# Performance work log

Measured on AMD Instinct MI355X. Metric: run time of the kernel, lower is better.

Reference implementation:

```python
import jax, jax.numpy as jnp
import numpy as np

D_MODEL, N_HEADS, D_LATENT = 1024, 16, 256
HEAD_DIM = D_MODEL // N_HEADS
B, T = 2, 2048


def apply_rope(x):
    # x: [B, T, H, D]
    Tn, D = x.shape[1], x.shape[3]
    inv_freq = 1.0 / (10000.0 ** (jnp.arange(0, D, 2, dtype=jnp.float32) / D))
    t = jnp.arange(Tn, dtype=jnp.float32)
    freqs = jnp.outer(t, inv_freq)               # [T, D/2]
    sin_f = jnp.sin(freqs)[None, :, None, :]
    cos_f = jnp.cos(freqs)[None, :, None, :]
    x1, x2 = jnp.split(x, 2, axis=-1)
    return jnp.concatenate([x1 * cos_f - x2 * sin_f,
                            x1 * sin_f + x2 * cos_f], axis=-1)


def setup_inputs() -> dict:
    key = jax.random.key(0)
    ks = jax.random.split(key, 5)
    s = lambda fan_in: 1.0 / np.sqrt(fan_in)
    return {
        "x": jax.random.normal(ks[0], (B, T, D_MODEL), jnp.float32),
        "Wq": jax.random.normal(ks[1], (D_MODEL, D_MODEL), jnp.float32) * s(D_MODEL),
        "bq": jnp.zeros((D_MODEL,), jnp.float32),
        "Wkv_down": jax.random.normal(ks[2], (D_MODEL, D_LATENT), jnp.float32) * s(D_MODEL),
        "bkv_down": jnp.zeros((D_LATENT,), jnp.float32),
        "Wkv_up": jax.random.normal(ks[3], (D_LATENT, 2 * D_MODEL), jnp.float32) * s(D_LATENT),
        "bkv_up": jnp.zeros((2 * D_MODEL,), jnp.float32),
        "Wo": jax.random.normal(ks[4], (D_MODEL, D_MODEL), jnp.float32) * s(D_MODEL),
        "bo": jnp.zeros((D_MODEL,), jnp.float32),
    }


def reference(x, Wq, bq, Wkv_down, bkv_down, Wkv_up, bkv_up, Wo, bo):
    Bn, Tn = x.shape[0], x.shape[1]
    q = x @ Wq + bq                              # [B, T, d_model]
    kv = (x @ Wkv_down + bkv_down) @ Wkv_up + bkv_up  # [B, T, 2*d_model]
    q = q.reshape(Bn, Tn, N_HEADS, HEAD_DIM)
    kv = kv.reshape(Bn, Tn, N_HEADS, 2 * HEAD_DIM)
    k, v = jnp.split(kv, 2, axis=-1)
    q = apply_rope(q)
    k = apply_rope(k)
    q = q.transpose(0, 2, 1, 3)                  # [B, H, T, D]
    k = k.transpose(0, 2, 1, 3)
    v = v.transpose(0, 2, 1, 3)

    att = jnp.einsum('bhqd,bhkd->bhqk', q, k) / jnp.sqrt(jnp.float32(HEAD_DIM))

    idx = jnp.arange(Tn, dtype=jnp.float32)
    dist_signed = idx[:, None] - idx[None, :]    # [T, T]
    log_sparse = -0.1 * jnp.log(jnp.abs(dist_signed) + 1.0)
    decay = jnp.exp(-jnp.maximum(dist_signed, 0.0) * 0.01)
    att = att + (log_sparse + jnp.log(decay + 1e-9))[None, None]
    att = jax.nn.softmax(att, axis=-1)
    out = jnp.einsum('bhqk,bhkd->bhqd', att, v)  # [B, H, T, D]

    # Infini/memory branch: mean-pooled single-slot attention
    memory_k = jnp.mean(k, axis=2, keepdims=True)  # [B, H, 1, D]
    memory_v = jnp.mean(v, axis=2, keepdims=True)
    memory_scores = jnp.einsum('bhqd,bhkd->bhqk', q, memory_k)  # [B, H, T, 1]
    infini_out = jax.nn.sigmoid(memory_scores) * memory_v       # [B, H, T, D]
    out = out + 0.2 * infini_out

    out = out.transpose(0, 2, 1, 3).reshape(Bn, Tn, D_MODEL)
    return out @ Wo + bo
```

## Files before the change

### kernel.cpp

```cpp
#include <hip/hip_runtime.h>
#include <hip/hip_bf16.h>

#define D_MODEL 1024
#define N_HEADS 16
#define HEAD_DIM 64
#define D_LATENT 256
#define BATCH 2
#define SEQ 2048
#define M_ROWS (BATCH * SEQ)

typedef __bf16 bf16;
typedef __attribute__((ext_vector_type(4))) __bf16 bf16x4;
typedef __attribute__((ext_vector_type(8))) __bf16 bf16x8;
typedef __attribute__((ext_vector_type(4))) float f32x4;

#define MFMA_BF16(a, b, c) __builtin_amdgcn_mfma_f32_16x16x32_bf16((a), (b), (c), 0, 0, 0)
#define LOG2E 1.4426950408889634f
#define SBAR() __builtin_amdgcn_s_barrier()
#define SCHED0() __builtin_amdgcn_sched_barrier(0)

__device__ __forceinline__ void gll16(const void* g, void* l) {
    __builtin_amdgcn_global_load_lds(
        (const __attribute__((address_space(1))) unsigned int*)g,
        (__attribute__((address_space(3))) unsigned int*)l, 16, 0, 0);
}
__device__ __forceinline__ void vwait4() { asm volatile("s_waitcnt vmcnt(4)" ::: "memory"); }
__device__ __forceinline__ void vwait0() { asm volatile("s_waitcnt vmcnt(0)" ::: "memory"); }

__device__ __forceinline__ void tw_body(
    const float* __restrict__ W, bf16* __restrict__ Wt, int K, int N,
    int b, float (*tw)[33], int tid)
{
    int nx = N / 32;
    int n0 = (b % nx) * 32, k0 = (b / nx) * 32;
    int c = tid & 31, r = tid >> 5;
    #pragma unroll
    for (int it = 0; it < 4; ++it)
        tw[r + it * 8][c] = W[(size_t)(k0 + r + it * 8) * N + n0 + c];
    __syncthreads();
    #pragma unroll
    for (int it = 0; it < 4; ++it)
        Wt[(size_t)(n0 + r + it * 8) * K + k0 + c] = (bf16)tw[c][r + it * 8];
}

__global__ __launch_bounds__(256) void prep_all(
    const float* __restrict__ x, bf16* __restrict__ xb,
    const float* __restrict__ Wq, bf16* __restrict__ Wqt,
    const float* __restrict__ Wd, bf16* __restrict__ Wdt,
    const float* __restrict__ Wu, bf16* __restrict__ Wut,
    const float* __restrict__ Wo, bf16* __restrict__ Wot,
    float2* __restrict__ rtab, float* __restrict__ bias2,
    float* __restrict__ memb)
{
    __shared__ float tw[32][33];
    const int bid = blockIdx.x, tid = threadIdx.x;
    if (bid < 2048) {
        int i = bid * 256 + tid;
        const float4* s = ((const float4*)x) + (size_t)i * 2;
        float4 a = s[0], b = s[1];
        bf16x8 v;
        v[0] = (bf16)a.x; v[1] = (bf16)a.y; v[2] = (bf16)a.z; v[3] = (bf16)a.w;
        v[4] = (bf16)b.x; v[5] = (bf16)b.y; v[6] = (bf16)b.z; v[7] = (bf16)b.w;
        *(bf16x8*)(xb + (size_t)i * 8) = v;
    } else if (bid < 3072) {
        tw_body(Wq, Wqt, 1024, 1024, bid - 2048, tw, tid);
    } else if (bid < 3328) {
        tw_body(Wd, Wdt, 1024, 256, bid - 3072, tw, tid);
    } else if (bid < 3840) {
        tw_body(Wu, Wut, 256, 2048, bid - 3328, tw, tid);
    } else if (bid < 4864) {
        tw_body(Wo, Wot, 1024, 1024, bid - 3840, tw, tid);
    } else if (bid < 5120) {
        int i = (bid - 4864) * 256 + tid;
        int j = i & 31, t = i >> 5;
        float inv_freq = exp2f((float)j * -0.4152410118609203f);
        float ang = (float)t * inv_freq;
        float sn, cs; sincosf(ang, &sn, &cs);
        rtab[i] = make_float2(cs, sn);
    } else {
        int i = (bid - 5120) * 256 + tid;
        if (i < 2 * SEQ - 1) {
            float d = (float)(i - (SEQ - 1));
            float ls  = -0.1f * logf(fabsf(d) + 1.0f);
            float dec = expf(-fmaxf(d, 0.0f) * 0.01f);
            bias2[i] = (ls + logf(dec + 1e-9f)) * LOG2E;
        }
        if (i < 4096) memb[i] = 0.f;
    }
}

__device__ __forceinline__ void stage_gemm(
    const bf16* __restrict__ A, const bf16* __restrict__ Bt, int K, int k0,
    bf16* As, bf16* Bs, int m0, int n0, int tid)
{
    #pragma unroll
    for (int it = 0; it < 2; ++it) {
        int c = it * 256 + tid;
        int row = c >> 2, part = c & 3;
        int p = part ^ ((row >> 1) & 3);
        gll16(A  + (size_t)(m0 + row) * K + k0 + p * 8, As + c * 8);
        gll16(Bt + (size_t)(n0 + row) * K + k0 + p * 8, Bs + c * 8);
    }
}

__device__ __forceinline__ void gemm_body(
    const bf16* __restrict__ A, const bf16* __restrict__ Bt, int K,
    bf16* sh, f32x4 (&acc)[4][4],
    int m0, int n0, int tid, int l15, int lh, int wr, int wc)
{
    stage_gemm(A, Bt, K, 0, sh, sh + 8192, m0, n0, tid);
    int cur = 0;
    for (int k0 = 0; k0 < K; k0 += 32) {
        if (k0 + 32 < K) {
            stage_gemm(A, Bt, K, k0 + 32, sh + (cur ^ 1) * 4096,
                       sh + 8192 + (cur ^ 1) * 4096, m0, n0, tid);
            vwait4();
        } else {
            vwait0();
        }
        SCHED0(); SBAR(); SCHED0();
        const bf16* As = sh + cur * 4096;
        const bf16* Bs = sh + 8192 + cur * 4096;
        bf16x8 af[4], bg[4];
        #pragma unroll
        for (int i = 0; i < 4; ++i) {
            int row = wr * 64 + i * 16 + l15;
            int cc = lh ^ ((row >> 1) & 3);
            af[i] = *(const bf16x8*)(As + row * 32 + cc * 8);
        }
        #pragma unroll
        for (int j = 0; j < 4; ++j) {
            int row = wc * 64 + j * 16 + l15;
            int cc = lh ^ ((row >> 1) & 3);
            bg[j] = *(const bf16x8*)(Bs + row * 32 + cc * 8);
        }
        #pragma unroll
        for (int i = 0; i < 4; ++i)
            #pragma unroll
            for (int j = 0; j < 4; ++j)
                acc[i][j] = MFMA_BF16(af[i], bg[j], acc[i][j]);
        SCHED0(); SBAR(); SCHED0();
        cur ^= 1;
    }
}

__global__ __launch_bounds__(256) void gemm_qkvd(
    const bf16* __restrict__ xb,
    const bf16* __restrict__ Wqt, const float* __restrict__ bq,
    const float2* __restrict__ rtab, bf16* __restrict__ Qh,
    const bf16* __restrict__ Wdt, const float* __restrict__ bkvd,
    bf16* __restrict__ kvd)
{
    __shared__ bf16 sh[16384];
    const int tid = threadIdx.x, lane = tid & 63, w = tid >> 6;
    const int wr = w >> 1, wc = w & 1;
    const int l15 = lane & 15, lh = lane >> 4;
    const int bx = blockIdx.x;
    const int m0 = blockIdx.y * 128;
    const bf16* Bt = (bx < 8) ? Wqt : Wdt;
    const int n0 = (bx < 8) ? bx * 128 : (bx - 8) * 128;

    f32x4 acc[4][4] = {};
    gemm_body(xb, Bt, D_MODEL, sh, acc, m0, n0, tid, l15, lh, wr, wc);

    if (bx < 8) {
        const int head = bx * 2 + wc;
        #pragma unroll
        for (int i = 0; i < 4; ++i) {
            #pragma unroll
            for (int r = 0; r < 4; ++r) {
                int m = m0 + wr * 64 + i * 16 + lh * 4 + r;
                int tpos = m & (SEQ - 1), b = m >> 11;
                bf16* orow = Qh + ((size_t)(b * N_HEADS + head) * SEQ + tpos) * 64;
                #pragma unroll
                for (int j01 = 0; j01 < 2; ++j01) {
                    int jj = j01 * 16 + l15;
                    float2 cssn = rtab[tpos * 32 + jj];
                    float v1 = acc[i][j01][r]     + bq[head * 64 + jj];
                    float v2 = acc[i][j01 + 2][r] + bq[head * 64 + jj + 32];
                    orow[jj]      = (bf16)(v1 * cssn.x - v2 * cssn.y);
                    orow[jj + 32] = (bf16)(v1 * cssn.y + v2 * cssn.x);
                }
            }
        }
    } else {
        #pragma unroll
        for (int i = 0; i < 4; ++i) {
            int row = m0 + wr * 64 + i * 16 + lh * 4;
            #pragma unroll
            for (int j = 0; j < 4; ++j) {
                int col = n0 + wc * 64 + j * 16 + l15;
                float bv = bkvd[col];
                #pragma unroll
                for (int r = 0; r < 4; ++r)
                    kvd[(size_t)(row + r) * D_LATENT + col] = (bf16)(acc[i][j][r] + bv);
            }
        }
    }
}

__global__ __launch_bounds__(256) void gemm_kv_rope(
    const bf16* __restrict__ A, const bf16* __restrict__ Bt,
    const float* __restrict__ bias, const float2* __restrict__ rtab,
    bf16* __restrict__ Kh, bf16* __restrict__ Vt, float* __restrict__ memb)
{
    __shared__ bf16 sh[16384];
    const int tid = threadIdx.x, lane = tid & 63, w = tid >> 6;
    const int wr = w >> 1, wc = w & 1;
    const int l15 = lane & 15, lh = lane >> 4;
    const int head = blockIdx.x;
    const int m0 = blockIdx.y * 128;
    const int b = m0 >> 11;
    const int bh = b * N_HEADS + head;
    const int tpos0 = m0 & (SEQ - 1);

    f32x4 acc[4][4] = {};
    gemm_body(A, Bt, D_LATENT, sh, acc, m0, head * 128, tid, l15, lh, wr, wc);

    if (wc == 0) {
        float s0 = 0.f, s1 = 0.f, s2 = 0.f, s3 = 0.f;
        #pragma unroll
        for (int i = 0; i < 4; ++i) {
            #pragma unroll
            for (int r = 0; r < 4; ++r) {
                int m = m0 + wr * 64 + i * 16 + lh * 4 + r;
                int tpos = m & (SEQ - 1);
                bf16* orow = Kh + ((size_t)bh * SEQ + tpos) * 64;
                float2 ca = rtab[tpos * 32 + l15];
                float v1 = acc[i][0][r] + bias[head * 128 + l15];
                float v2 = acc[i][2][r] + bias[head * 128 + l15 + 32];
                float o1 = v1 * ca.x - v2 * ca.y;
                float o2 = v1 * ca.y + v2 * ca.x;
                orow[l15]      = (bf16)o1;
                orow[l15 + 32] = (bf16)o2;
                float2 cb = rtab[tpos * 32 + 16 + l15];
                float v3 = acc[i][1][r] + bias[head * 128 + 16 + l15];
                float v4 = acc[i][3][r] + bias[head * 128 + 48 + l15];
                float o3 = v3 * cb.x - v4 * cb.y;
                float o4 = v3 * cb.y + v4 * cb.x;
                orow[16 + l15] = (bf16)o3;
                orow[48 + l15] = (bf16)o4;
                s0 += o1; s1 += o3; s2 += o2; s3 += o4;
            }
        }
        s0 += __shfl_xor(s0, 16, 64); s0 += __shfl_xor(s0, 32, 64);
        s1 += __shfl_xor(s1, 16, 64); s1 += __shfl_xor(s1, 32, 64);
        s2 += __shfl_xor(s2, 16, 64); s2 += __shfl_xor(s2, 32, 64);
        s3 += __shfl_xor(s3, 16, 64); s3 += __shfl_xor(s3, 32, 64);
        if (lane < 16) {
            const float sc = 1.f / SEQ;
            atomicAdd(&memb[bh * 128 + l15],      s0 * sc);
            atomicAdd(&memb[bh * 128 + 16 + l15], s1 * sc);
            atomicAdd(&memb[bh * 128 + 32 + l15], s2 * sc);
            atomicAdd(&memb[bh * 128 + 48 + l15], s3 * sc);
        }
    } else {
        float sv[4] = {};
        #pragma unroll
        for (int i = 0; i < 4; ++i) {
            #pragma unroll
            for (int j = 0; j < 4; ++j) {
                int d = j * 16 + l15;
                float bv = bias[head * 128 + 64 + d];
                #pragma unroll
                for (int r = 0; r < 4; ++r) {
                    int t = wr * 64 + i * 16 + lh * 4 + r;
                    float v = acc[i][j][r] + bv;
                    sh[d * 136 + t] = (bf16)v;
                    sv[j] += v;
                }
            }
        }
        #pragma unroll
        for (int j = 0; j < 4; ++j) {
            sv[j] += __shfl_xor(sv[j], 16, 64);
            sv[j] += __shfl_xor(sv[j], 32, 64);
        }
        if (lane < 16) {
            const float sc = 1.f / SEQ;
            #pragma unroll
            for (int j = 0; j < 4; ++j)
                atomicAdd(&memb[bh * 128 + 64 + j * 16 + l15], sv[j] * sc);
        }
    }
    __syncthreads();
    {
        int d = tid >> 2, seg = tid & 3;
        bf16* dst = Vt + ((size_t)bh * 64 + d) * SEQ + tpos0 + seg * 32;
        #pragma unroll
        for (int e = 0; e < 4; ++e)
            *(bf16x8*)(dst + e * 8) = *(const bf16x8*)(sh + d * 136 + seg * 32 + e * 8);
    }
}

__global__ __launch_bounds__(256) void gemm_out(
    const bf16* __restrict__ A, const bf16* __restrict__ Bt,
    const float* __restrict__ bias, float* __restrict__ C)
{
    __shared__ bf16 sh[16384];
    const int tid = threadIdx.x, lane = tid & 63, w = tid >> 6;
    const int wr = w >> 1, wc = w & 1;
    const int l15 = lane & 15, lh = lane >> 4;
    const int m0 = blockIdx.y * 128, n0 = blockIdx.x * 128;
    f32x4 acc[4][4] = {};
    gemm_body(A, Bt, D_MODEL, sh, acc, m0, n0, tid, l15, lh, wr, wc);

    #pragma unroll
    for (int i = 0; i < 4; ++i) {
        int row = m0 + wr * 64 + i * 16 + lh * 4;
        #pragma unroll
        for (int j = 0; j < 4; ++j) {
            int col = n0 + wc * 64 + j * 16 + l15;
            float bv = bias[col];
            #pragma unroll
            for (int r = 0; r < 4; ++r)
                C[(size_t)(row + r) * D_MODEL + col] = acc[i][j][r] + bv;
        }
    }
}

__global__ __launch_bounds__(256) void attn_mfma(
    const bf16* __restrict__ Qh,
    const bf16* __restrict__ Kh,
    const bf16* __restrict__ Vt,
    const float* __restrict__ bias2,
    const float* __restrict__ memkv,
    bf16* __restrict__ ao)
{
    __shared__ bf16 PQ[4 * 16 * 88];
    __shared__ bf16 Ks[2 * 64 * 64];
    __shared__ bf16 Vs[2 * 64 * 64];
    __shared__ float bias_s[2112];

    const int tid = threadIdx.x;
    const int lane = tid & 63;
    const int w = tid >> 6;
    const int l15 = lane & 15, lh = lane >> 4;
    const int bh = blockIdx.y;
    const int q0 = blockIdx.x * 64;
    const size_t bhT = (size_t)bh * SEQ;

    for (int i = tid; i < 2111; i += 256) bias_s[i] = bias2[q0 + i];
    #pragma unroll
    for (int it = 0; it < 2; ++it) {
        int c = it * 256 + tid;
        int row = c >> 3, part = c & 7;
        int p = part ^ (row & 7);
        gll16(Qh + (bhT + q0 + row) * 64 + p * 8, PQ + c * 8);
    }
    #pragma unroll
    for (int it = 0; it < 2; ++it) {
        int c = it * 256 + tid;
        int row = c >> 3, part = c & 7;
        int p = part ^ (row & 7);
        gll16(Kh + (bhT + row) * 64 + p * 8, Ks + c * 8);
        gll16(Vt + ((size_t)bh * 64 + row) * SEQ + p * 8, Vs + c * 8);
    }
    __syncthreads();

    const int qrow = w * 16 + l15;
    bf16x8 qf[2];
    #pragma unroll
    for (int ks = 0; ks < 2; ++ks) {
        int pp = (ks * 4 + lh) ^ (qrow & 7);
        qf[ks] = *(const bf16x8*)(PQ + qrow * 64 + pp * 8);
    }

    const float* mk = memkv + bh * 128;
    float di = 0.f;
    #pragma unroll
    for (int ks = 0; ks < 2; ++ks)
        #pragma unroll
        for (int e = 0; e < 8; ++e)
            di += (float)qf[ks][e] * mk[ks * 32 + lh * 8 + e];
    di += __shfl_xor(di, 16, 64);
    di += __shfl_xor(di, 32, 64);

    f32x4 o[4] = {};
    float lsum = 0.f;
    bf16* Psw = PQ + w * 16 * 88;
    int cur = 0;

    for (int kt = 0; kt < SEQ / 64; ++kt) {
        if (kt < SEQ / 64 - 1) {
            #pragma unroll
            for (int it = 0; it < 2; ++it) {
                int c = it * 256 + tid;
                int row = c >> 3, part = c & 7;
                int p = part ^ (row & 7);
                gll16(Kh + (bhT + (kt + 1) * 64 + row) * 64 + p * 8,
                      Ks + (cur ^ 1) * 4096 + c * 8);
                gll16(Vt + ((size_t)bh * 64 + row) * SEQ + (kt + 1) * 64 + p * 8,
                      Vs + (cur ^ 1) * 4096 + c * 8);
            }
            vwait4();
        } else {
            vwait0();
        }
        SCHED0(); SBAR(); SCHED0();
        const bf16* Kc = Ks + cur * 4096;
        const bf16* Vc = Vs + cur * 4096;

        f32x4 s_[4] = {};
        #pragma unroll
        for (int ks = 0; ks < 2; ++ks) {
            #pragma unroll
            for (int jk = 0; jk < 4; ++jk) {
                int row = jk * 16 + l15;
                int cc = (ks * 4 + lh) ^ (row & 7);
                bf16x8 kf = *(const bf16x8*)(Kc + row * 64 + cc * 8);
                s_[jk] = MFMA_BF16(kf, qf[ks], s_[jk]);
            }
        }

        #pragma unroll
        for (int jk = 0; jk < 4; ++jk) {
            int idx0 = (w * 16 + l15) - (kt * 64 + jk * 16 + lh * 4) + 2047;
            bf16x4 pb;
            #pragma unroll
            for (int r = 0; r < 4; ++r) {
                float pexp = exp2f(s_[jk][r] * (0.125f * LOG2E) + bias_s[idx0 - r]);
                lsum += pexp;
                pb[r] = (bf16)pexp;
            }
            *(bf16x4*)(Psw + l15 * 88 + jk * 16 + lh * 4) = pb;
        }

        #pragma unroll
        for (int ks = 0; ks < 2; ++ks) {
            bf16x8 pf = *(const bf16x8*)(Psw + l15 * 88 + ks * 32 + lh * 8);
            #pragma unroll
            for (int jd = 0; jd < 4; ++jd) {
                int row = jd * 16 + l15;
                int cc = (ks * 4 + lh) ^ (row & 7);
                bf16x8 vf = *(const bf16x8*)(Vc + row * 64 + cc * 8);
                o[jd] = MFMA_BF16(pf, vf, o[jd]);
            }
        }
        SCHED0(); SBAR(); SCHED0();
        cur ^= 1;
    }

    lsum += __shfl_xor(lsum, 16, 64);
    lsum += __shfl_xor(lsum, 32, 64);

    float inv_l[4], sig[4];
    #pragma unroll
    for (int r = 0; r < 4; ++r) {
        int src = lh * 4 + r;
        inv_l[r] = 1.f / __shfl(lsum, src, 64);
        float dd = __shfl(di, src, 64);
        sig[r] = 1.f / (1.f + __expf(-dd));
    }

    const int b = bh >> 4, h = bh & 15;
    #pragma unroll
    for (int jd = 0; jd < 4; ++jd) {
        int d = jd * 16 + l15;
        float mv = mk[64 + d];
        #pragma unroll
        for (int r = 0; r < 4; ++r) {
            int qi = q0 + w * 16 + lh * 4 + r;
            float val = o[jd][r] * inv_l[r] + 0.2f * sig[r] * mv;
            ao[((size_t)(b * SEQ + qi)) * D_MODEL + h * 64 + d] = (bf16)val;
        }
    }
}

extern "C" void kernel_launch(void* const* d_in, const int* in_sizes, int n_in,
                              void* d_out, int out_size, void* d_ws, size_t ws_size,
                              hipStream_t stream)
{
    const float* x        = (const float*)d_in[0];
    const float* Wq       = (const float*)d_in[1];
    const float* bq       = (const float*)d_in[2];
    const float* Wkv_down = (const float*)d_in[3];
    const float* bkv_down = (const float*)d_in[4];
    const float* Wkv_up   = (const float*)d_in[5];
    const float* bkv_up   = (const float*)d_in[6];
    const float* Wo       = (const float*)d_in[7];
    const float* bo       = (const float*)d_in[8];
    float* out = (float*)d_out;

    char* p = (char*)d_ws;
    bf16* xb   = (bf16*)p;  p += 8388608;
    bf16* Wqt  = (bf16*)p;  p += 2097152;
    bf16* Wdt  = (bf16*)p;  p += 524288;
    bf16* Wut  = (bf16*)p;  p += 1048576;
    bf16* Wot  = (bf16*)p;  p += 2097152;
    bf16* kvd  = (bf16*)p;  p += 2097152;
    bf16* Qh   = (bf16*)p;  p += 8388608;
    bf16* Kh   = (bf16*)p;  p += 8388608;
    bf16* Vt   = (bf16*)p;  p += 8388608;
    bf16* ao   = (bf16*)p;  p += 8388608;
    float* memb  = (float*)p; p += 16384;
    float* bias2 = (float*)p; p += 16384;
    float2* rtab = (float2*)p; p += 524288;

    dim3 blk(256);

    prep_all<<<dim3(5136), blk, 0, stream>>>(
        x, xb, Wq, Wqt, Wkv_down, Wdt, Wkv_up, Wut, Wo, Wot, rtab, bias2, memb);

    gemm_qkvd<<<dim3(10, M_ROWS / 128), blk, 0, stream>>>(
        xb, Wqt, bq, rtab, Qh, Wdt, bkv_down, kvd);

    gemm_kv_rope<<<dim3(N_HEADS, M_ROWS / 128), blk, 0, stream>>>(
        kvd, Wut, bkv_up, rtab, Kh, Vt, memb);

    attn_mfma<<<dim3(SEQ / 64, BATCH * N_HEADS), blk, 0, stream>>>(
        Qh, Kh, Vt, bias2, memb, ao);

    gemm_out<<<dim3(D_MODEL / 128, M_ROWS / 128), blk, 0, stream>>>(
        ao, Wot, bo, out);
}
```

Baseline: 223.0 us.

## Rework attention with 32x32 MFMA, register-resident P and smaller remapped blocks

The attention kernel switches from 16x16x32 to 32x32x16 bf16 MFMA, with 128-thread blocks where each wave owns 32 query rows. The softmax probabilities now stay in registers and are exchanged between half-waves with cross-lane shuffles, instead of making a round trip through a shared-memory P buffer. Blocks are remapped onto a 1D grid that interleaves heads, and s_setprio is raised around the MFMA sections. In exchange, the K/V double buffering and its prefetch overlap are dropped: each tile is loaded and then a full barrier is taken, so latency hiding now depends on having more resident blocks.

Result: faster. 218.4 us (-2.1%).

```diff
diff --git a/kernel.cpp b/kernel.cpp
--- a/kernel.cpp
+++ b/kernel.cpp
@@ -13,8 +13,10 @@
 typedef __attribute__((ext_vector_type(4))) __bf16 bf16x4;
 typedef __attribute__((ext_vector_type(8))) __bf16 bf16x8;
 typedef __attribute__((ext_vector_type(4))) float f32x4;
+typedef __attribute__((ext_vector_type(16))) float f32x16;
 
 #define MFMA_BF16(a, b, c) __builtin_amdgcn_mfma_f32_16x16x32_bf16((a), (b), (c), 0, 0, 0)
+#define MFMA32(a, b, c)    __builtin_amdgcn_mfma_f32_32x32x16_bf16((a), (b), (c), 0, 0, 0)
 #define LOG2E 1.4426950408889634f
 #define SBAR() __builtin_amdgcn_s_barrier()
 #define SCHED0() __builtin_amdgcn_sched_barrier(0)
@@ -319,7 +321,7 @@
     }
 }
 
-__global__ __launch_bounds__(256) void attn_mfma(
+__global__ __launch_bounds__(128) void attn_mfma(
     const bf16* __restrict__ Qh,
     const bf16* __restrict__ Kh,
     const bf16* __restrict__ Vt,
@@ -327,142 +329,138 @@
     const float* __restrict__ memkv,
     bf16* __restrict__ ao)
 {
-    __shared__ bf16 PQ[4 * 16 * 88];
-    __shared__ bf16 Ks[2 * 64 * 64];
-    __shared__ bf16 Vs[2 * 64 * 64];
+    __shared__ bf16 KV[8192];
     __shared__ float bias_s[2112];
 
     const int tid = threadIdx.x;
     const int lane = tid & 63;
     const int w = tid >> 6;
-    const int l15 = lane & 15, lh = lane >> 4;
-    const int bh = blockIdx.y;
-    const int q0 = blockIdx.x * 64;
+    const int l31 = lane & 31, h5 = lane >> 5;
+    const int B = blockIdx.x;
+    const int loc = B >> 3;
+    const int bh = (B & 7) * 4 + (loc >> 5);
+    const int q0 = (loc & 31) * 64;
     const size_t bhT = (size_t)bh * SEQ;
-
-    for (int i = tid; i < 2111; i += 256) bias_s[i] = bias2[q0 + i];
-    #pragma unroll
-    for (int it = 0; it < 2; ++it) {
-        int c = it * 256 + tid;
+    const int b = bh >> 4, h = bh & 15;
+
+    for (int i = tid; i < 2111; i += 128) bias_s[i] = bias2[q0 + i];
+    #pragma unroll
+    for (int it = 0; it < 4; ++it) {
+        int c = it * 128 + tid;
         int row = c >> 3, part = c & 7;
         int p = part ^ (row & 7);
-        gll16(Qh + (bhT + q0 + row) * 64 + p * 8, PQ + c * 8);
-    }
-    #pragma unroll
-    for (int it = 0; it < 2; ++it) {
-        int c = it * 256 + tid;
-        int row = c >> 3, part = c & 7;
-        int p = part ^ (row & 7);
-        gll16(Kh + (bhT + row) * 64 + p * 8, Ks + c * 8);
-        gll16(Vt + ((size_t)bh * 64 + row) * SEQ + p * 8, Vs + c * 8);
+        gll16(Qh + (bhT + q0 + row) * 64 + p * 8, KV + c * 8);
     }
     __syncthreads();
 
-    const int qrow = w * 16 + l15;
-    bf16x8 qf[2];
-    #pragma unroll
-    for (int ks = 0; ks < 2; ++ks) {
-        int pp = (ks * 4 + lh) ^ (qrow & 7);
-        qf[ks] = *(const bf16x8*)(PQ + qrow * 64 + pp * 8);
-    }
-
+    const int qrow = w * 32 + l31;
+    bf16x8 qf[4];
+    #pragma unroll
+    for (int kg = 0; kg < 4; ++kg) {
+        int pp = (kg * 2 + h5) ^ (qrow & 7);
+        qf[kg] = *(const bf16x8*)(KV + qrow * 64 + pp * 8);
+    }
     const float* mk = memkv + bh * 128;
     float di = 0.f;
     #pragma unroll
-    for (int ks = 0; ks < 2; ++ks)
+    for (int kg = 0; kg < 4; ++kg)
         #pragma unroll
         for (int e = 0; e < 8; ++e)
-            di += (float)qf[ks][e] * mk[ks * 32 + lh * 8 + e];
-    di += __shfl_xor(di, 16, 64);
+            di += (float)qf[kg][e] * mk[kg * 16 + h5 * 8 + e];
     di += __shfl_xor(di, 32, 64);
-
-    f32x4 o[4] = {};
+    __syncthreads();
+
+    bf16* Ks = KV;
+    bf16* Vs = KV + 4096;
+    f32x16 o0 = {}, o1 = {};
     float lsum = 0.f;
-    bf16* Psw = PQ + w * 16 * 88;
-    int cur = 0;
+    const float C1 = 0.125f * LOG2E;
 
     for (int kt = 0; kt < SEQ / 64; ++kt) {
-        if (kt < SEQ / 64 - 1) {
-            #pragma unroll
-            for (int it = 0; it < 2; ++it) {
-                int c = it * 256 + tid;
-                int row = c >> 3, part = c & 7;
-                int p = part ^ (row & 7);
-                gll16(Kh + (bhT + (kt + 1) * 64 + row) * 64 + p * 8,
-                      Ks + (cur ^ 1) * 4096 + c * 8);
-                gll16(Vt + ((size_t)bh * 64 + row) * SEQ + (kt + 1) * 64 + p * 8,
-                      Vs + (cur ^ 1) * 4096 + c * 8);
+        #pragma unroll
+        for (int it = 0; it < 4; ++it) {
+            int c = it * 128 + tid;
+            int row = c >> 3, part = c & 7;
+            int p = part ^ (row & 7);
+            gll16(Kh + (bhT + kt * 64 + row) * 64 + p * 8, Ks + c * 8);
+            gll16(Vt + ((size_t)bh * 64 + row) * SEQ + kt * 64 + p * 8, Vs + c * 8);
+        }
+        __syncthreads();
+
+        f32x16 s0 = {}, s1 = {};
+        __builtin_amdgcn_s_setprio(1);
+        #pragma unroll
+        for (int kg = 0; kg < 4; ++kg) {
+            int pp = (kg * 2 + h5) ^ (l31 & 7);
+            bf16x8 kf0 = *(const bf16x8*)(Ks + l31 * 64 + pp * 8);
+            bf16x8 kf1 = *(const bf16x8*)(Ks + (32 + l31) * 64 + pp * 8);
+            s0 = MFMA32(kf0, qf[kg], s0);
+            s1 = MFMA32(kf1, qf[kg], s1);
+        }
+        __builtin_amdgcn_s_setprio(0);
+
+        uint2 qd[8];
+        auto mkquads = [&](const f32x16& sg, int g) {
+            #pragma unroll
+            for (int rq = 0; rq < 4; ++rq) {
+                int base = kt * 64 + g * 32 + rq * 8 + h5 * 4;
+                int bidx = (w * 32 + l31) - base + 2047;
+                union { bf16x4 v; uint2 u; } pk;
+                #pragma unroll
+                for (int j = 0; j < 4; ++j) {
+                    float pe = exp2f(sg[rq * 4 + j] * C1 + bias_s[bidx - j]);
+                    lsum += pe;
+                    pk.v[j] = (bf16)pe;
+                }
+                qd[g * 4 + rq] = pk.u;
             }
-            vwait4();
-        } else {
-            vwait0();
-        }
-        SCHED0(); SBAR(); SCHED0();
-        const bf16* Kc = Ks + cur * 4096;
-        const bf16* Vc = Vs + cur * 4096;
-
-        f32x4 s_[4] = {};
-        #pragma unroll
-        for (int ks = 0; ks < 2; ++ks) {
-            #pragma unroll
-            for (int jk = 0; jk < 4; ++jk) {
-                int row = jk * 16 + l15;
-                int cc = (ks * 4 + lh) ^ (row & 7);
-                bf16x8 kf = *(const bf16x8*)(Kc + row * 64 + cc * 8);
-                s_[jk] = MFMA_BF16(kf, qf[ks], s_[jk]);
-            }
-        }
-
-        #pragma unroll
-        for (int jk = 0; jk < 4; ++jk) {
-            int idx0 = (w * 16 + l15) - (kt * 64 + jk * 16 + lh * 4) + 2047;
-            bf16x4 pb;
-            #pragma unroll
-            for (int r = 0; r < 4; ++r) {
-                float pexp = exp2f(s_[jk][r] * (0.125f * LOG2E) + bias_s[idx0 - r]);
-                lsum += pexp;
-                pb[r] = (bf16)pexp;
-            }
-            *(bf16x4*)(Psw + l15 * 88 + jk * 16 + lh * 4) = pb;
-        }
-
-        #pragma unroll
-        for (int ks = 0; ks < 2; ++ks) {
-            bf16x8 pf = *(const bf16x8*)(Psw + l15 * 88 + ks * 32 + lh * 8);
-            #pragma unroll
-            for (int jd = 0; jd < 4; ++jd) {
-                int row = jd * 16 + l15;
-                int cc = (ks * 4 + lh) ^ (row & 7);
-                bf16x8 vf = *(const bf16x8*)(Vc + row * 64 + cc * 8);
-                o[jd] = MFMA_BF16(pf, vf, o[jd]);
-            }
-        }
-        SCHED0(); SBAR(); SCHED0();
-        cur ^= 1;
-    }
-
-    lsum += __shfl_xor(lsum, 16, 64);
+        };
+        mkquads(s0, 0);
+        mkquads(s1, 1);
+
+        #pragma unroll
+        for (int c = 0; c < 4; ++c) {
+            uint2 own = h5 ? qd[2 * c + 1] : qd[2 * c];
+            uint2 sup = h5 ? qd[2 * c]     : qd[2 * c + 1];
+            uint2 rec;
+            rec.x = (unsigned)__shfl_xor((int)sup.x, 32, 64);
+            rec.y = (unsigned)__shfl_xor((int)sup.y, 32, 64);
+            uint2 lo = h5 ? rec : own;
+            uint2 hi = h5 ? own : rec;
+            union { unsigned u[4]; bf16x8 v; } pa;
+            pa.u[0] = lo.x; pa.u[1] = lo.y; pa.u[2] = hi.x; pa.u[3] = hi.y;
+            int pp = (c * 2 + h5) ^ (l31 & 7);
+            bf16x8 vf0 = *(const bf16x8*)(Vs + l31 * 64 + pp * 8);
+            bf16x8 vf1 = *(const bf16x8*)(Vs + (32 + l31) * 64 + pp * 8);
+            __builtin_amdgcn_s_setprio(1);
+            o0 = MFMA32(pa.v, vf0, o0);
+            o1 = MFMA32(pa.v, vf1, o1);
+            __builtin_amdgcn_s_setprio(0);
+        }
+        __syncthreads();
+    }
+
     lsum += __shfl_xor(lsum, 32, 64);
-
-    float inv_l[4], sig[4];
-    #pragma unroll
-    for (int r = 0; r < 4; ++r) {
-        int src = lh * 4 + r;
-        inv_l[r] = 1.f / __shfl(lsum, src, 64);
-        float dd = __shfl(di, src, 64);
-        sig[r] = 1.f / (1.f + __expf(-dd));
-    }
-
-    const int b = bh >> 4, h = bh & 15;
-    #pragma unroll
-    for (int jd = 0; jd < 4; ++jd) {
-        int d = jd * 16 + l15;
-        float mv = mk[64 + d];
-        #pragma unroll
-        for (int r = 0; r < 4; ++r) {
-            int qi = q0 + w * 16 + lh * 4 + r;
-            float val = o[jd][r] * inv_l[r] + 0.2f * sig[r] * mv;
-            ao[((size_t)(b * SEQ + qi)) * D_MODEL + h * 64 + d] = (bf16)val;
+    float* inv_s = bias_s;
+    float* sig_s = bias_s + 64;
+    if (h5 == 0) {
+        inv_s[qrow] = 1.f / lsum;
+        sig_s[qrow] = 1.f / (1.f + __expf(-di));
+    }
+    float mv0 = mk[64 + l31], mv1 = mk[96 + l31];
+    #pragma unroll
+    for (int rq = 0; rq < 4; ++rq) {
+        #pragma unroll
+        for (int j = 0; j < 4; ++j) {
+            int qr = w * 32 + j + rq * 8 + h5 * 4;
+            float il = inv_s[qr];
+            float sg = sig_s[qr];
+            int qi = q0 + qr;
+            float v0 = o0[rq * 4 + j] * il + 0.2f * sg * mv0;
+            float v1 = o1[rq * 4 + j] * il + 0.2f * sg * mv1;
+            bf16* op = ao + ((size_t)(b * SEQ + qi)) * D_MODEL + h * 64;
+            op[l31]      = (bf16)v0;
+            op[32 + l31] = (bf16)v1;
         }
     }
 }
@@ -508,7 +506,7 @@
     gemm_kv_rope<<<dim3(N_HEADS, M_ROWS / 128), blk, 0, stream>>>(
         kvd, Wut, bkv_up, rtab, Kh, Vt, memb);
 
-    attn_mfma<<<dim3(SEQ / 64, BATCH * N_HEADS), blk, 0, stream>>>(
+    attn_mfma<<<dim3(1024), dim3(128), 0, stream>>>(
         Qh, Kh, Vt, bias2, memb, ao);
 
     gemm_out<<<dim3(D_MODEL / 128, M_ROWS / 128), blk, 0, stream>>>(
```
